# Kernel optimization log

Measured on AMD Instinct MI355X. Metric: run time of the kernel, lower is better.

Reference implementation:

```python
import jax, jax.numpy as jnp
import numpy as np

T, B, D, H, L = 128, 256, 1024, 1024, 512  # seq_len, batch, input_size, hidden_size, latent(mlp_size)


def setup_inputs() -> dict:
    key = jax.random.key(0)
    ks = jax.random.split(key, 12)
    s = 0.05
    return {
        "sen_t": jax.random.normal(ks[0], (T, B, D), jnp.float32),
        "eps": jax.random.normal(ks[1], (T, B, L), jnp.float32),
        "Wq": jax.random.normal(ks[2], (D, D), jnp.float32) * s,
        "bq": jnp.zeros((D,), jnp.float32),
        "Wqmu": jax.random.normal(ks[3], (D, L), jnp.float32) * s,
        "bqmu": jnp.zeros((L,), jnp.float32),
        "Wqvar": jax.random.normal(ks[4], (D, L), jnp.float32) * s,
        "bqvar": jnp.zeros((L,), jnp.float32),
        "Wp": jax.random.normal(ks[5], (H, D), jnp.float32) * s,
        "bp": jnp.zeros((D,), jnp.float32),
        "Wpmu": jax.random.normal(ks[6], (D, L), jnp.float32) * s,
        "bpmu": jnp.zeros((L,), jnp.float32),
        "Wpvar": jax.random.normal(ks[7], (D, L), jnp.float32) * s,
        "bpvar": jnp.zeros((L,), jnp.float32),
        "Wx": jax.random.normal(ks[8], (D, H), jnp.float32) * s,
        "bx": jnp.zeros((H,), jnp.float32),
        "W_ih": jax.random.normal(ks[9], (4 * H, H), jnp.float32) * s,
        "b_ih": jnp.zeros((4 * H,), jnp.float32),
        "W_hh": jax.random.normal(ks[10], (4 * H, H), jnp.float32) * s,
        "b_hh": jnp.zeros((4 * H,), jnp.float32),
    }


def reference(sen_t, eps, Wq, bq, Wqmu, bqmu, Wqvar, bqvar, Wp, bp, Wpmu, bpmu,
              Wpvar, bpvar, Wx, bx, W_ih, b_ih, W_hh, b_hh):
    batch = sen_t.shape[1]
    hid = W_hh.shape[1]

    def step(carry, inp):
        h, c = carry
        s, e = inp
        # posterior branch: q_i = lin_q(sen_t[i])
        q = jax.nn.relu(s @ Wq + bq)                      # [B, D]
        q_mu = q @ Wqmu + bqmu                            # [B, L]
        q_logvar = jnp.log(jax.nn.softplus(q @ Wqvar + bqvar))
        z = q_mu + e * jnp.exp(0.5 * q_logvar)            # reparameterization
        # prior branch: p_i = lin_p(h_i)
        p = jax.nn.relu(h @ Wp + bp)                      # [B, D]
        p_mu = p @ Wpmu + bpmu
        p_logvar = jnp.log(jax.nn.softplus(p @ Wpvar + bpvar))
        kl = jnp.sum(0.5 * (p_logvar - q_logvar
                            + (jnp.exp(q_logvar) + (q_mu - p_mu) ** 2) / jnp.exp(p_logvar)
                            - 1.0), axis=-1)              # [B]
        # lin_x + LSTMCell
        x = jax.nn.relu(q @ Wx + bx)                      # [B, H]
        gates = x @ W_ih.T + b_ih + h @ W_hh.T + b_hh     # [B, 4H]
        i_g, f_g, g_g, o_g = jnp.split(gates, 4, axis=-1)
        c_new = jax.nn.sigmoid(f_g) * c + jax.nn.sigmoid(i_g) * jnp.tanh(g_g)
        h_new = jax.nn.sigmoid(o_g) * jnp.tanh(c_new)
        return (h_new, c_new), (z, kl)

    h0 = jnp.zeros((batch, hid), sen_t.dtype)
    (_, _), (z, kl) = jax.lax.scan(step, (h0, h0), (sen_t, eps))
    return z, kl  # [T,B,L], [T,B]
```

## Files before the change

kernel.cpp:

```cpp
#include <hip/hip_runtime.h>
#include <hip/hip_cooperative_groups.h>


typedef __attribute__((ext_vector_type(8))) short short8;
typedef __attribute__((ext_vector_type(4))) float f32x4;
typedef unsigned short u16;
typedef unsigned int u32;

__device__ __forceinline__ u16 f2b(float f) {
  u32 x = __float_as_uint(f);
  u32 r = (x + 0x7fffu + ((x >> 16) & 1u)) >> 16;
  return (u16)r;
}
__device__ __forceinline__ float b2f(u16 u) {
  return __uint_as_float(((u32)u) << 16);
}

__device__ __forceinline__ void gl_lds16(const void* g, void* l) {
  using GT = __attribute__((address_space(1))) const unsigned int;
  using LT = __attribute__((address_space(3))) unsigned int;
  __builtin_amdgcn_global_load_lds((GT*)g, (LT*)l, 16, 0, 0);
}

__device__ __forceinline__ f32x4 mfma_bf16(short8 a, short8 b, f32x4 c) {
  asm("v_mfma_f32_16x16x32_bf16 %0, %1, %2, %0" : "+v"(c) : "v"(a), "v"(b));
  return c;
}


__global__ void conv_bf16_k(const float4* __restrict__ in, uint2* __restrict__ out, int n4) {
  for (int i = blockIdx.x * blockDim.x + threadIdx.x; i < n4; i += gridDim.x * blockDim.x) {
    float4 v = in[i];
    uint2 o;
    o.x = (u32)f2b(v.x) | ((u32)f2b(v.y) << 16);
    o.y = (u32)f2b(v.z) | ((u32)f2b(v.w) << 16);
    out[i] = o;
  }
}

__global__ void transpose_bf16_k(const float* __restrict__ in, u16* __restrict__ out, int R, int C) {
  __shared__ float tile[32][33];
  int c0 = blockIdx.x * 32, r0 = blockIdx.y * 32;
  int tx = threadIdx.x, ty = threadIdx.y;
#pragma unroll
  for (int i = 0; i < 4; ++i)
    tile[ty + i * 8][tx] = in[(long)(r0 + ty + i * 8) * C + c0 + tx];
  __syncthreads();
#pragma unroll
  for (int i = 0; i < 4; ++i)
    out[(long)(c0 + ty + i * 8) * R + r0 + tx] = f2b(tile[tx][ty + i * 8]);
}

__global__ void gather_gates_k(const float4* __restrict__ in, u16* __restrict__ out) {
  int n = blockIdx.x;
  int t = threadIdx.x;
  int src = ((n >> 4) & 3) * 1024 + (n >> 6) * 16 + (n & 15);
  float4 v = in[(long)src * 256 + t];
  u16* o = out + (long)n * 1024 + t * 4;
  o[0] = f2b(v.x); o[1] = f2b(v.y); o[2] = f2b(v.z); o[3] = f2b(v.w);
}

__global__ void gate_bias_k(const float* __restrict__ bih, const float* __restrict__ bhh,
                            float* __restrict__ o) {
  int n = blockIdx.x * blockDim.x + threadIdx.x;
  int src = ((n >> 4) & 3) * 1024 + (n >> 6) * 16 + (n & 15);
  o[n] = bih[src] + bhh[src];
}

__global__ void concat_bias_k(const float* __restrict__ a, const float* __restrict__ b,
                              float* __restrict__ o, int n) {
  int i = blockIdx.x * blockDim.x + threadIdx.x;
  if (i < n) { o[i] = a[i]; o[n + i] = b[i]; }
}


template <bool RELU>
__global__ __launch_bounds__(256) void gemm_bt(
    const u16* __restrict__ A, const u16* __restrict__ BT, const float* __restrict__ bias,
    char* p0, char* p1, char* p2, int t1, int t2, int K, int N) {
  __shared__ char smem[32768];
  const int tid = threadIdx.x, lane = tid & 63, wid = tid >> 6;
  const int m0 = blockIdx.y * 128, n0 = blockIdx.x * 128;
  const int wm = wid >> 1, wn = wid & 1;

  const int c0 = wid * 64 + lane;
  const int srow = c0 >> 3;
  const int sk8 = (c0 & 7) * 16;
  const char* aG = (const char*)A + (long)(m0 + srow) * K * 2 + sk8;
  const char* bG = (const char*)BT + (long)(n0 + srow) * K * 2 + sk8;
  const long rstride = (long)K * 64;
  char* ldsA = smem;
  char* ldsB = smem + 16384;

  const int aoff = (wm * 64 + (lane & 15)) * 128 + (lane >> 4) * 16;
  const int boff = 16384 + (wn * 64 + (lane & 15)) * 128 + (lane >> 4) * 16;

  f32x4 acc[4][4];
#pragma unroll
  for (int i = 0; i < 4; ++i)
#pragma unroll
    for (int j = 0; j < 4; ++j) acc[i][j] = (f32x4){0.f, 0.f, 0.f, 0.f};

  const int nkt = K >> 6;
  for (int kt = 0; kt < nkt; ++kt) {
    __syncthreads();
#pragma unroll
    for (int r = 0; r < 4; ++r) {
      gl_lds16(aG + r * rstride + kt * 128, ldsA + (r * 4 + wid) * 1024);
      gl_lds16(bG + r * rstride + kt * 128, ldsB + (r * 4 + wid) * 1024);
    }
    __syncthreads();
#pragma unroll
    for (int kk = 0; kk < 2; ++kk) {
      short8 a[4], b[4];
#pragma unroll
      for (int i = 0; i < 4; ++i) a[i] = *(const short8*)(smem + aoff + i * 2048 + kk * 64);
#pragma unroll
      for (int j = 0; j < 4; ++j) b[j] = *(const short8*)(smem + boff + j * 2048 + kk * 64);
#pragma unroll
      for (int i = 0; i < 4; ++i)
#pragma unroll
        for (int j = 0; j < 4; ++j) acc[i][j] = mfma_bf16(a[i], b[j], acc[i][j]);
    }
  }

#pragma unroll
  for (int i = 0; i < 4; ++i) {
    int r4 = m0 + wm * 64 + i * 16 + (lane >> 4) * 4;
#pragma unroll
    for (int rr = 0; rr < 4; ++rr) {
      int R = r4 + rr;
      char* orow = (R < t1) ? (p0 + (long)R * N * 2)
                            : ((R < t2) ? (p1 + (long)(R - t1) * N * 2)
                                        : (p2 + (long)(R - t2) * N * 2));
#pragma unroll
      for (int j = 0; j < 4; ++j) {
        int col = n0 + wn * 64 + j * 16 + (lane & 15);
        float v = acc[i][j][rr] + bias[col];
        if (RELU) v = fmaxf(v, 0.f);
        ((u16*)orow)[col] = f2b(v);
      }
    }
  }
}


__global__ void z_k(const u16* __restrict__ QMV, const float* __restrict__ eps,
                    float* __restrict__ out) {
  long idx = (long)blockIdx.x * 256 + threadIdx.x;
  int row = (int)(idx >> 9), l = (int)(idx & 511);
  float qmu = b2f(QMV[(long)row * 1024 + l]);
  float qraw = b2f(QMV[(long)row * 1024 + 512 + l]);
  float sp = qraw > 15.f ? qraw : log1pf(expf(qraw));
  out[idx] = qmu + eps[idx] * sqrtf(sp);
}

__global__ void kl_k(const u16* __restrict__ QMV, const u16* __restrict__ PMV,
                     float* __restrict__ out) {
  int row = blockIdx.x * 4 + (threadIdx.x >> 6);
  int lane = threadIdx.x & 63;
  const u16* qr = QMV + (long)row * 1024;
  const u16* pr = PMV + (long)row * 1024;
  float s = 0.f;
#pragma unroll
  for (int i = 0; i < 8; ++i) {
    int l = lane + i * 64;
    float qmu = b2f(qr[l]), qraw = b2f(qr[512 + l]);
    float pmu = b2f(pr[l]), praw = b2f(pr[512 + l]);
    float spq = qraw > 15.f ? qraw : log1pf(expf(qraw));
    float spp = praw > 15.f ? praw : log1pf(expf(praw));
    float d = qmu - pmu;
    s += logf(spp) - logf(spq) + (spq + d * d) / spp - 1.f;
  }
#pragma unroll
  for (int m = 32; m >= 1; m >>= 1) s += __shfl_xor(s, m, 64);
  if (lane == 0) out[row] = 0.5f * s;
}


__global__ __launch_bounds__(512) void vae_loop_k(
    const u16* __restrict__ WcatT, u16* h0buf, u16* h1buf,
    const char* xg0, const char* xg1, const char* xg2,
    u16* __restrict__ Pb, const float* __restrict__ bp) {
  extern __shared__ char smem[];
  const int tid = threadIdx.x, lane = tid & 63, wid = tid >> 6;
  const int blk = blockIdx.x, mh = blk & 1, nt = blk >> 1;
  const int n0 = nt * 64, m0 = mh * 128;

  {
    const char* src = (const char*)(WcatT + (long)n0 * 1024);
#pragma unroll
    for (int r = 0; r < 16; ++r) {
      int cb = (r * 8 + wid) * 64;
      gl_lds16(src + (long)(cb + lane) * 16, smem + (long)cb * 16);
    }
  }
  {
    u32* hp = (u32*)h0buf;
    for (int i = blk * 512 + tid; i < 131072; i += 160 * 512) hp[i] = 0u;
  }
  __syncthreads();
  cooperative_groups::this_grid().sync();

  const int u = lane & 15;
  const int kc = (lane >> 4) * 16;
  const long a_off = (long)(m0 + wid * 16 + u) * 2048 + kc;
  const int boff0 = (0 * 16 + u) * 2048 + kc;
  const int boff1 = (1 * 16 + u) * 2048 + kc;
  const int boff2 = (2 * 16 + u) * 2048 + kc;
  const int boff3 = (3 * 16 + u) * 2048 + kc;
  const int myr = m0 + wid * 16 + (lane >> 4) * 4;
  const bool gate = (n0 < 4096);
  float bpj[4];
  if (!gate) {
#pragma unroll
    for (int j = 0; j < 4; ++j) bpj[j] = bp[(n0 - 4096) + j * 16 + u];
  }
  float creg[4] = {0.f, 0.f, 0.f, 0.f};

  for (int t = 0; t < 128; ++t) {
    const char* Ab = (const char*)((t & 1) ? h1buf : h0buf) + a_off;
    u16* hn = (t & 1) ? h0buf : h1buf;
    f32x4 acc0 = (f32x4){0,0,0,0}, acc1 = (f32x4){0,0,0,0};
    f32x4 acc2 = (f32x4){0,0,0,0}, acc3 = (f32x4){0,0,0,0};
#pragma unroll 4
    for (int ks = 0; ks < 32; ++ks) {
      short8 a = *(const short8*)(Ab + ks * 64);
      short8 b0 = *(const short8*)(smem + boff0 + ks * 64);
      short8 b1 = *(const short8*)(smem + boff1 + ks * 64);
      short8 b2 = *(const short8*)(smem + boff2 + ks * 64);
      short8 b3 = *(const short8*)(smem + boff3 + ks * 64);
      acc0 = mfma_bf16(a, b0, acc0);
      acc1 = mfma_bf16(a, b1, acc1);
      acc2 = mfma_bf16(a, b2, acc2);
      acc3 = mfma_bf16(a, b3, acc3);
    }
    if (gate) {
      const char* xgb;
      if (t < 64)      xgb = xg0 + (long)t * 256 * 8192;
      else if (t < 96) xgb = xg1 + (long)(t - 64) * 256 * 8192;
      else             xgb = xg2 + (long)(t - 96) * 256 * 8192;
#pragma unroll
      for (int rr = 0; rr < 4; ++rr) {
        int R = myr + rr;
        const u16* xr = (const u16*)(xgb + (long)R * 8192) + n0 + u;
        float G0 = acc0[rr] + b2f(xr[0]);
        float G1 = acc1[rr] + b2f(xr[16]);
        float G2 = acc2[rr] + b2f(xr[32]);
        float G3 = acc3[rr] + b2f(xr[48]);
        float ai = 1.f / (1.f + expf(-G0));
        float af = 1.f / (1.f + expf(-G1));
        float ag = tanhf(G2);
        float ao = 1.f / (1.f + expf(-G3));
        float cn = af * creg[rr] + ai * ag;
        creg[rr] = cn;
        float hv = ao * tanhf(cn);
        hn[(long)R * 1024 + nt * 16 + u] = f2b(hv);
      }
    } else {
#pragma unroll
      for (int rr = 0; rr < 4; ++rr) {
        int R = myr + rr;
        u16* prow = Pb + ((long)t * 256 + R) * 1024 + (n0 - 4096) + u;
        prow[0]  = f2b(fmaxf(acc0[rr] + bpj[0], 0.f));
        prow[16] = f2b(fmaxf(acc1[rr] + bpj[1], 0.f));
        prow[32] = f2b(fmaxf(acc2[rr] + bpj[2], 0.f));
        prow[48] = f2b(fmaxf(acc3[rr] + bpj[3], 0.f));
      }
    }
    cooperative_groups::this_grid().sync();
  }
}


extern "C" void kernel_launch(void* const* d_in, const int* in_sizes, int n_in,
                              void* d_out, int out_size, void* d_ws, size_t ws_size,
                              hipStream_t stream) {
  const float* sen   = (const float*)d_in[0];
  const float* eps   = (const float*)d_in[1];
  const float* Wq    = (const float*)d_in[2];
  const float* bq    = (const float*)d_in[3];
  const float* Wqmu  = (const float*)d_in[4];
  const float* bqmu  = (const float*)d_in[5];
  const float* Wqvar = (const float*)d_in[6];
  const float* bqvar = (const float*)d_in[7];
  const float* Wp    = (const float*)d_in[8];
  const float* bp    = (const float*)d_in[9];
  const float* Wpmu  = (const float*)d_in[10];
  const float* bpmu  = (const float*)d_in[11];
  const float* Wpvar = (const float*)d_in[12];
  const float* bpvar = (const float*)d_in[13];
  const float* Wx    = (const float*)d_in[14];
  const float* bx    = (const float*)d_in[15];
  const float* Wih   = (const float*)d_in[16];
  const float* bih   = (const float*)d_in[17];
  const float* Whh   = (const float*)d_in[18];
  const float* bhh   = (const float*)d_in[19];

  char* ws = (char*)d_ws;
  size_t off = 0;
  auto take = [&](size_t bytes) {
    char* p = ws + off;
    off += (bytes + 255) & ~(size_t)255;
    return p;
  };
  char* R1   = take(67108864);
  char* Qb   = take(67108864);
  char* QMVb = take(67108864);
  char* XGt  = take(67108864);
  u16* WqT   = (u16*)take(1024 * 1024 * 2);
  u16* WqmvT = (u16*)take(1024 * 1024 * 2);
  u16* WxT   = (u16*)take(1024 * 1024 * 2);
  u16* WihgT = (u16*)take((size_t)4096 * 1024 * 2);
  u16* WcatT = (u16*)take((size_t)5120 * 1024 * 2);
  u16* WpmvT = (u16*)take(1024 * 1024 * 2);
  float* bg   = (float*)take(4096 * 4);
  float* bqmv = (float*)take(1024 * 4);
  float* bpmv = (float*)take(1024 * 4);
  u16* h0 = (u16*)take(524288);
  u16* h1 = (u16*)take(524288);
  if (off > ws_size) return;

  char* xg0 = (char*)d_in[0];
  char* xg1 = (char*)d_in[1];
  char* xg2 = XGt;
  const int BIG = 1 << 30;

  conv_bf16_k<<<dim3(4096), dim3(256), 0, stream>>>((const float4*)sen, (uint2*)R1, 8388608);

  dim3 tb(32, 8);
  transpose_bf16_k<<<dim3(32, 32), tb, 0, stream>>>(Wq, WqT, 1024, 1024);
  transpose_bf16_k<<<dim3(16, 32), tb, 0, stream>>>(Wqmu, WqmvT, 1024, 512);
  transpose_bf16_k<<<dim3(16, 32), tb, 0, stream>>>(Wqvar, WqmvT + 512 * 1024, 1024, 512);
  transpose_bf16_k<<<dim3(32, 32), tb, 0, stream>>>(Wx, WxT, 1024, 1024);
  transpose_bf16_k<<<dim3(32, 32), tb, 0, stream>>>(Wp, WcatT + (size_t)4096 * 1024, 1024, 1024);
  transpose_bf16_k<<<dim3(16, 32), tb, 0, stream>>>(Wpmu, WpmvT, 1024, 512);
  transpose_bf16_k<<<dim3(16, 32), tb, 0, stream>>>(Wpvar, WpmvT + 512 * 1024, 1024, 512);

  gather_gates_k<<<dim3(4096), dim3(256), 0, stream>>>((const float4*)Wih, WihgT);
  gather_gates_k<<<dim3(4096), dim3(256), 0, stream>>>((const float4*)Whh, WcatT);
  gate_bias_k<<<dim3(16), dim3(256), 0, stream>>>(bih, bhh, bg);
  concat_bias_k<<<dim3(2), dim3(256), 0, stream>>>(bqmu, bqvar, bqmv, 512);
  concat_bias_k<<<dim3(2), dim3(256), 0, stream>>>(bpmu, bpvar, bpmv, 512);

  gemm_bt<true><<<dim3(8, 256), dim3(256), 0, stream>>>(
      (const u16*)R1, WqT, bq, Qb, Qb, Qb, BIG, BIG, 1024, 1024);
  gemm_bt<false><<<dim3(8, 256), dim3(256), 0, stream>>>(
      (const u16*)Qb, WqmvT, bqmv, QMVb, QMVb, QMVb, BIG, BIG, 1024, 1024);
  z_k<<<dim3(65536), dim3(256), 0, stream>>>((const u16*)QMVb, eps, (float*)d_out);
  gemm_bt<true><<<dim3(8, 256), dim3(256), 0, stream>>>(
      (const u16*)Qb, WxT, bx, R1, R1, R1, BIG, BIG, 1024, 1024);
  gemm_bt<false><<<dim3(32, 256), dim3(256), 0, stream>>>(
      (const u16*)R1, WihgT, bg, xg0, xg1, xg2, 16384, 24576, 1024, 4096);

  hipFuncSetAttribute((const void*)vae_loop_k, hipFuncAttributeMaxDynamicSharedMemorySize, 131072);
  u16* Pb = (u16*)R1;
  {
    void* args[] = {(void*)&WcatT, (void*)&h0, (void*)&h1, (void*)&xg0,
                    (void*)&xg1,  (void*)&xg2, (void*)&Pb, (void*)&bp};
    hipLaunchCooperativeKernel((void*)vae_loop_k, dim3(160), dim3(512), args, 131072, stream);
  }

  gemm_bt<false><<<dim3(8, 256), dim3(256), 0, stream>>>(
      (const u16*)R1, WpmvT, bpmv, XGt, XGt, XGt, BIG, BIG, 1024, 1024);
  kl_k<<<dim3(8192), dim3(256), 0, stream>>>((const u16*)QMVb, (const u16*)XGt,
                                             (float*)d_out + 16777216);
}
```

Measured before the change: 5.889 ms.

## Swizzle LDS layouts, halve loop-kernel waves, prefetch gate inputs, use fast transcendentals

The bf16 GEMM now writes LDS tiles with an XOR swizzle on the 16-byte chunk index and reads them back with the matching swizzle, aiming to avoid bank conflicts. The cooperative recurrent kernel goes from 512 to 256 threads per block. Each wave now computes 32 rows, so every B fragment read from LDS feeds two MFMAs, and the weight tile in LDS uses the same XOR swizzle. The precomputed input-gate values for the next timestep are loaded into registers before the grid barrier, taking that global-load latency off the critical path. Sigmoid and tanh switch to __expf-based forms, which cost fewer instructions but are slightly less accurate and use more registers per thread.

```diff
diff --git a/kernel.cpp b/kernel.cpp
--- a/kernel.cpp
+++ b/kernel.cpp
@@ -25,6 +25,11 @@
 __device__ __forceinline__ f32x4 mfma_bf16(short8 a, short8 b, f32x4 c) {
   asm("v_mfma_f32_16x16x32_bf16 %0, %1, %2, %0" : "+v"(c) : "v"(a), "v"(b));
   return c;
+}
+
+__device__ __forceinline__ float sigm(float x) { return 1.f / (1.f + __expf(-x)); }
+__device__ __forceinline__ float tanh_f(float x) {
+  return 1.f - 2.f / (__expf(2.f * x) + 1.f);
 }
 
 
@@ -85,15 +90,14 @@
 
   const int c0 = wid * 64 + lane;
   const int srow = c0 >> 3;
-  const int sk8 = (c0 & 7) * 16;
+  const int sk8 = (((lane & 7) ^ ((lane >> 3) & 7)) << 4);
   const char* aG = (const char*)A + (long)(m0 + srow) * K * 2 + sk8;
   const char* bG = (const char*)BT + (long)(n0 + srow) * K * 2 + sk8;
   const long rstride = (long)K * 64;
   char* ldsA = smem;
   char* ldsB = smem + 16384;
 
-  const int aoff = (wm * 64 + (lane & 15)) * 128 + (lane >> 4) * 16;
-  const int boff = 16384 + (wn * 64 + (lane & 15)) * 128 + (lane >> 4) * 16;
+  const int e = lane & 7;
 
   f32x4 acc[4][4];
 #pragma unroll
@@ -114,9 +118,17 @@
     for (int kk = 0; kk < 2; ++kk) {
       short8 a[4], b[4];
 #pragma unroll
-      for (int i = 0; i < 4; ++i) a[i] = *(const short8*)(smem + aoff + i * 2048 + kk * 64);
-#pragma unroll
-      for (int j = 0; j < 4; ++j) b[j] = *(const short8*)(smem + boff + j * 2048 + kk * 64);
+      for (int i = 0; i < 4; ++i) {
+        int row = wm * 64 + i * 16 + (lane & 15);
+        int ch = (kk * 4 + (lane >> 4)) ^ e;
+        a[i] = *(const short8*)(smem + row * 128 + (ch << 4));
+      }
+#pragma unroll
+      for (int j = 0; j < 4; ++j) {
+        int row = wn * 64 + j * 16 + (lane & 15);
+        int ch = (kk * 4 + (lane >> 4)) ^ e;
+        b[j] = *(const short8*)(smem + 16384 + row * 128 + (ch << 4));
+      }
 #pragma unroll
       for (int i = 0; i < 4; ++i)
 #pragma unroll
@@ -178,7 +190,7 @@
 }
 
 
-__global__ __launch_bounds__(512) void vae_loop_k(
+__global__ __launch_bounds__(256) void vae_loop_k(
     const u16* __restrict__ WcatT, u16* h0buf, u16* h1buf,
     const char* xg0, const char* xg1, const char* xg2,
     u16* __restrict__ Pb, const float* __restrict__ bp) {
@@ -186,87 +198,125 @@
   const int tid = threadIdx.x, lane = tid & 63, wid = tid >> 6;
   const int blk = blockIdx.x, mh = blk & 1, nt = blk >> 1;
   const int n0 = nt * 64, m0 = mh * 128;
+  const int u = lane & 15, q = lane >> 4, e = lane & 7;
 
   {
     const char* src = (const char*)(WcatT + (long)n0 * 1024);
 #pragma unroll
-    for (int r = 0; r < 16; ++r) {
-      int cb = (r * 8 + wid) * 64;
-      gl_lds16(src + (long)(cb + lane) * 16, smem + (long)cb * 16);
+    for (int it = 0; it < 32; ++it) {
+      int d = it * 256 + tid;
+      int row = d >> 7, c = d & 127;
+      gl_lds16(src + (long)row * 2048 + ((c ^ (row & 7)) << 4), smem + (long)d * 16);
     }
   }
   {
     u32* hp = (u32*)h0buf;
-    for (int i = blk * 512 + tid; i < 131072; i += 160 * 512) hp[i] = 0u;
-  }
-  __syncthreads();
-  cooperative_groups::this_grid().sync();
-
-  const int u = lane & 15;
-  const int kc = (lane >> 4) * 16;
-  const long a_off = (long)(m0 + wid * 16 + u) * 2048 + kc;
-  const int boff0 = (0 * 16 + u) * 2048 + kc;
-  const int boff1 = (1 * 16 + u) * 2048 + kc;
-  const int boff2 = (2 * 16 + u) * 2048 + kc;
-  const int boff3 = (3 * 16 + u) * 2048 + kc;
-  const int myr = m0 + wid * 16 + (lane >> 4) * 4;
+    for (int i = blk * 256 + tid; i < 131072; i += 160 * 256) hp[i] = 0u;
+  }
+
   const bool gate = (n0 < 4096);
   float bpj[4];
   if (!gate) {
 #pragma unroll
     for (int j = 0; j < 4; ++j) bpj[j] = bp[(n0 - 4096) + j * 16 + u];
   }
-  float creg[4] = {0.f, 0.f, 0.f, 0.f};
+
+  long aoff0 = (long)(m0 + wid * 32 + u) * 2048 + q * 16;
+  long aoff1 = aoff0 + 16 * 2048;
+  int bbase0 = (0 * 16 + u) * 2048;
+  int bbase1 = (1 * 16 + u) * 2048;
+  int bbase2 = (2 * 16 + u) * 2048;
+  int bbase3 = (3 * 16 + u) * 2048;
+
+  float creg[8];
+#pragma unroll
+  for (int i = 0; i < 8; ++i) creg[i] = 0.f;
+
+  u32 xv[2][4][4];
+  if (gate) {
+    const u16* xr = (const u16*)xg0 + n0 + u;
+#pragma unroll
+    for (int i = 0; i < 2; ++i)
+#pragma unroll
+      for (int rr = 0; rr < 4; ++rr) {
+        const u16* p = xr + (long)(m0 + wid * 32 + i * 16 + q * 4 + rr) * 4096;
+#pragma unroll
+        for (int j = 0; j < 4; ++j) xv[i][rr][j] = p[j * 16];
+      }
+  }
+
+  __syncthreads();
+  cooperative_groups::this_grid().sync();
 
   for (int t = 0; t < 128; ++t) {
-    const char* Ab = (const char*)((t & 1) ? h1buf : h0buf) + a_off;
+    const char* Ab = (const char*)((t & 1) ? h1buf : h0buf);
     u16* hn = (t & 1) ? h0buf : h1buf;
-    f32x4 acc0 = (f32x4){0,0,0,0}, acc1 = (f32x4){0,0,0,0};
-    f32x4 acc2 = (f32x4){0,0,0,0}, acc3 = (f32x4){0,0,0,0};
-#pragma unroll 4
+    f32x4 acc[2][4];
+#pragma unroll
+    for (int i = 0; i < 2; ++i)
+#pragma unroll
+      for (int j = 0; j < 4; ++j) acc[i][j] = (f32x4){0.f, 0.f, 0.f, 0.f};
+
+#pragma unroll
     for (int ks = 0; ks < 32; ++ks) {
-      short8 a = *(const short8*)(Ab + ks * 64);
-      short8 b0 = *(const short8*)(smem + boff0 + ks * 64);
-      short8 b1 = *(const short8*)(smem + boff1 + ks * 64);
-      short8 b2 = *(const short8*)(smem + boff2 + ks * 64);
-      short8 b3 = *(const short8*)(smem + boff3 + ks * 64);
-      acc0 = mfma_bf16(a, b0, acc0);
-      acc1 = mfma_bf16(a, b1, acc1);
-      acc2 = mfma_bf16(a, b2, acc2);
-      acc3 = mfma_bf16(a, b3, acc3);
-    }
+      short8 a0 = *(const short8*)(Ab + aoff0 + ks * 64);
+      short8 a1 = *(const short8*)(Ab + aoff1 + ks * 64);
+      int ch = ((ks * 4 + q) ^ e) << 4;
+      short8 b0 = *(const short8*)(smem + bbase0 + ch);
+      short8 b1 = *(const short8*)(smem + bbase1 + ch);
+      short8 b2 = *(const short8*)(smem + bbase2 + ch);
+      short8 b3 = *(const short8*)(smem + bbase3 + ch);
+      acc[0][0] = mfma_bf16(a0, b0, acc[0][0]);
+      acc[1][0] = mfma_bf16(a1, b0, acc[1][0]);
+      acc[0][1] = mfma_bf16(a0, b1, acc[0][1]);
+      acc[1][1] = mfma_bf16(a1, b1, acc[1][1]);
+      acc[0][2] = mfma_bf16(a0, b2, acc[0][2]);
+      acc[1][2] = mfma_bf16(a1, b2, acc[1][2]);
+      acc[0][3] = mfma_bf16(a0, b3, acc[0][3]);
+      acc[1][3] = mfma_bf16(a1, b3, acc[1][3]);
+    }
+
     if (gate) {
-      const char* xgb;
-      if (t < 64)      xgb = xg0 + (long)t * 256 * 8192;
-      else if (t < 96) xgb = xg1 + (long)(t - 64) * 256 * 8192;
-      else             xgb = xg2 + (long)(t - 96) * 256 * 8192;
-#pragma unroll
-      for (int rr = 0; rr < 4; ++rr) {
-        int R = myr + rr;
-        const u16* xr = (const u16*)(xgb + (long)R * 8192) + n0 + u;
-        float G0 = acc0[rr] + b2f(xr[0]);
-        float G1 = acc1[rr] + b2f(xr[16]);
-        float G2 = acc2[rr] + b2f(xr[32]);
-        float G3 = acc3[rr] + b2f(xr[48]);
-        float ai = 1.f / (1.f + expf(-G0));
-        float af = 1.f / (1.f + expf(-G1));
-        float ag = tanhf(G2);
-        float ao = 1.f / (1.f + expf(-G3));
-        float cn = af * creg[rr] + ai * ag;
-        creg[rr] = cn;
-        float hv = ao * tanhf(cn);
-        hn[(long)R * 1024 + nt * 16 + u] = f2b(hv);
+#pragma unroll
+      for (int i = 0; i < 2; ++i)
+#pragma unroll
+        for (int rr = 0; rr < 4; ++rr) {
+          int R = m0 + wid * 32 + i * 16 + q * 4 + rr;
+          float G0 = acc[i][0][rr] + b2f((u16)xv[i][rr][0]);
+          float G1 = acc[i][1][rr] + b2f((u16)xv[i][rr][1]);
+          float G2 = acc[i][2][rr] + b2f((u16)xv[i][rr][2]);
+          float G3 = acc[i][3][rr] + b2f((u16)xv[i][rr][3]);
+          float cn = sigm(G1) * creg[i * 4 + rr] + sigm(G0) * tanh_f(G2);
+          creg[i * 4 + rr] = cn;
+          hn[(long)R * 1024 + nt * 16 + u] = f2b(sigm(G3) * tanh_f(cn));
+        }
+      if (t + 1 < 128) {
+        int tn = t + 1;
+        const char* xgb = (tn < 64) ? xg0 + (long)tn * 2097152
+                        : (tn < 96) ? xg1 + (long)(tn - 64) * 2097152
+                                    : xg2 + (long)(tn - 96) * 2097152;
+        const u16* xr = (const u16*)xgb + n0 + u;
+#pragma unroll
+        for (int i = 0; i < 2; ++i)
+#pragma unroll
+          for (int rr = 0; rr < 4; ++rr) {
+            const u16* p = xr + (long)(m0 + wid * 32 + i * 16 + q * 4 + rr) * 4096;
+#pragma unroll
+            for (int j = 0; j < 4; ++j) xv[i][rr][j] = p[j * 16];
+          }
       }
     } else {
 #pragma unroll
-      for (int rr = 0; rr < 4; ++rr) {
-        int R = myr + rr;
-        u16* prow = Pb + ((long)t * 256 + R) * 1024 + (n0 - 4096) + u;
-        prow[0]  = f2b(fmaxf(acc0[rr] + bpj[0], 0.f));
-        prow[16] = f2b(fmaxf(acc1[rr] + bpj[1], 0.f));
-        prow[32] = f2b(fmaxf(acc2[rr] + bpj[2], 0.f));
-        prow[48] = f2b(fmaxf(acc3[rr] + bpj[3], 0.f));
-      }
+      for (int i = 0; i < 2; ++i)
+#pragma unroll
+        for (int rr = 0; rr < 4; ++rr) {
+          int R = m0 + wid * 32 + i * 16 + q * 4 + rr;
+          u16* prow = Pb + ((long)t * 256 + R) * 1024 + (n0 - 4096) + u;
+          prow[0]  = f2b(fmaxf(acc[i][0][rr] + bpj[0], 0.f));
+          prow[16] = f2b(fmaxf(acc[i][1][rr] + bpj[1], 0.f));
+          prow[32] = f2b(fmaxf(acc[i][2][rr] + bpj[2], 0.f));
+          prow[48] = f2b(fmaxf(acc[i][3][rr] + bpj[3], 0.f));
+        }
     }
     cooperative_groups::this_grid().sync();
   }
@@ -358,7 +408,7 @@
   {
     void* args[] = {(void*)&WcatT, (void*)&h0, (void*)&h1, (void*)&xg0,
                     (void*)&xg1,  (void*)&xg2, (void*)&Pb, (void*)&bp};
-    hipLaunchCooperativeKernel((void*)vae_loop_k, dim3(160), dim3(512), args, 131072, stream);
+    hipLaunchCooperativeKernel((void*)vae_loop_k, dim3(160), dim3(256), args, 131072, stream);
   }
 
   gemm_bt<false><<<dim3(8, 256), dim3(256), 0, stream>>>(
```

Result: faster. 5.289 ms (-10.2%).
